# Kernel tuning notes

Hardware: AMD Instinct MI355X
Metric: run time of the kernel (lower is better)

## Reference

```python
import jax, jax.numpy as jnp
import numpy as np

N_NODES = 50000
N_EDGES = 800000
NODE_DIM = 256
EDGE_DIM = 64
NUM_REL = 4
HID = 512      # hidden_dims[0]
LAST = 128     # last_dim_size
BATCH = 16384
EPS = 1e-10    # torchdrug RelationalGraphConv degree-normalization eps


def _glorot(k, shape):
    fan_in = shape[-1]
    return jax.random.normal(k, shape, jnp.float32) / np.sqrt(fan_in).astype(np.float32)


def setup_inputs() -> dict:
    key = jax.random.key(0)
    ks = jax.random.split(key, 20)
    inp = {}
    inp["inputs"] = jax.random.randint(ks[0], (BATCH, 3), 0, N_NODES, dtype=jnp.int32)
    inp["node_feature"] = jax.random.normal(ks[1], (N_NODES, NODE_DIM), jnp.float32)
    inp["edge_feature"] = jax.random.normal(ks[2], (N_EDGES, EDGE_DIM), jnp.float32)
    inp["edge_src"] = jax.random.randint(ks[3], (N_EDGES,), 0, N_NODES, dtype=jnp.int32)
    inp["edge_dst"] = jax.random.randint(ks[4], (N_EDGES,), 0, N_NODES, dtype=jnp.int32)
    inp["edge_rel"] = jax.random.randint(ks[5], (N_EDGES,), 0, NUM_REL, dtype=jnp.int32)
    # RGCN layer 1: 256 -> 512
    inp["We1"] = _glorot(ks[6], (NODE_DIM, EDGE_DIM)); inp["be1"] = jnp.zeros((NODE_DIM,), jnp.float32)
    inp["Wl1"] = _glorot(ks[7], (HID, NUM_REL * NODE_DIM)); inp["bl1"] = jnp.zeros((HID,), jnp.float32)
    inp["Ws1"] = _glorot(ks[8], (HID, NODE_DIM)); inp["bs1"] = jnp.zeros((HID,), jnp.float32)
    # RGCN layer 2: 512 -> 128
    inp["We2"] = _glorot(ks[9], (HID, EDGE_DIM)); inp["be2"] = jnp.zeros((HID,), jnp.float32)
    inp["Wl2"] = _glorot(ks[10], (LAST, NUM_REL * HID)); inp["bl2"] = jnp.zeros((LAST,), jnp.float32)
    inp["Ws2"] = _glorot(ks[11], (LAST, HID)); inp["bs2"] = jnp.zeros((LAST,), jnp.float32)
    # ccle_mlp: edge_dim -> 256 -> 128
    inp["Wc1"] = _glorot(ks[12], (256, EDGE_DIM)); inp["bc1"] = jnp.zeros((256,), jnp.float32)
    inp["Wc2"] = _glorot(ks[13], (LAST, 256)); inp["bc2"] = jnp.zeros((LAST,), jnp.float32)
    # final MLP: 3*128 -> 128 -> 64 -> 1
    inp["Wf1"] = _glorot(ks[14], (128, 3 * LAST)); inp["bf1"] = jnp.zeros((128,), jnp.float32)
    inp["Wf2"] = _glorot(ks[15], (64, 128)); inp["bf2"] = jnp.zeros((64,), jnp.float32)
    inp["Wf3"] = _glorot(ks[16], (1, 64)); inp["bf3"] = jnp.zeros((1,), jnp.float32)
    return inp


def _rgcn_layer(x, edge_src, edge_dst, edge_rel, edge_feat, We, be, Wl, bl, Ws, bs):
    """torchdrug RelationalGraphConv: message = x[src] + edge_linear(edge_feat);
    per-(node,relation) mean aggregation; combine = linear(update) + self_loop(x); relu."""
    in_dim = x.shape[1]
    msg = x[edge_src] + edge_feat @ We.T + be                      # [E, in_dim]
    seg = edge_dst * NUM_REL + edge_rel                            # [E]
    agg = jax.ops.segment_sum(msg, seg, num_segments=N_NODES * NUM_REL)
    cnt = jax.ops.segment_sum(jnp.ones((msg.shape[0], 1), msg.dtype), seg,
                              num_segments=N_NODES * NUM_REL)
    upd = (agg / (cnt + EPS)).reshape(N_NODES, NUM_REL * in_dim)   # [N, R*in_dim]
    return jax.nn.relu(upd @ Wl.T + bl + x @ Ws.T + bs)


def reference(inputs, node_feature, edge_feature, edge_src, edge_dst, edge_rel,
              We1, be1, Wl1, bl1, Ws1, bs1,
              We2, be2, Wl2, bl2, Ws2, bs2,
              Wc1, bc1, Wc2, bc2,
              Wf1, bf1, Wf2, bf2, Wf3, bf3):
    d1, d2, ctx = inputs[:, 0], inputs[:, 1], inputs[:, 2]
    h = _rgcn_layer(node_feature, edge_src, edge_dst, edge_rel, edge_feature,
                    We1, be1, Wl1, bl1, Ws1, bs1)
    h = _rgcn_layer(h, edge_src, edge_dst, edge_rel, edge_feature,
                    We2, be2, Wl2, bl2, Ws2, bs2)
    x1 = h[d1]                                                     # [B, 128]
    x2 = h[d2]                                                     # [B, 128]
    ef = edge_feature[ctx]                                         # [B, 64]
    x3 = jax.nn.relu(ef @ Wc1.T + bc1) @ Wc2.T + bc2               # [B, 128]
    x = jnp.concatenate([x1, x2, x3], axis=1)                      # [B, 384]
    x = jax.nn.relu(x @ Wf1.T + bf1)
    x = jax.nn.relu(x @ Wf2.T + bf2)
    return x @ Wf3.T + bf3                                         # [B, 1]
```

## Files before the change

### kernel.cpp

```cpp
#include <hip/hip_runtime.h>
#include <hip/hip_bf16.h>

#define N_NODES 50000
#define N_EDGES 800000
#define NODE_DIM 256
#define EDGE_DIM 64
#define NUM_REL 4
#define HID 512
#define LAST 128
#define BATCH 16384
#define EPS 1e-10f
#define NSEG (N_NODES * NUM_REL)

#define K1 1600
#define K2 832

typedef __bf16 bf16_t;
typedef __attribute__((ext_vector_type(8))) __bf16 bf16x8;
typedef __attribute__((ext_vector_type(4))) __bf16 bf16x4;
typedef __attribute__((ext_vector_type(2))) __bf16 bf16x2;
typedef __attribute__((ext_vector_type(4))) float f32x4;

typedef __attribute__((address_space(1))) const unsigned int g_u32;
typedef __attribute__((address_space(3))) unsigned int l_u32;
static __device__ __forceinline__ void gload16(const void* g, void* l) {
    __builtin_amdgcn_global_load_lds((g_u32*)g, (l_u32*)l, 16, 0, 0);
}

__global__ __launch_bounds__(256) void hist_kernel(
    const int* __restrict__ edst, const int* __restrict__ erel, int* __restrict__ hist)
{
    int e = blockIdx.x * 256 + threadIdx.x;
    if (e >= N_EDGES) return;
    atomicAdd(&hist[edst[e] * NUM_REL + erel[e]], 1);
}

#define SCAN_B 2048
__global__ __launch_bounds__(256) void scan1(
    const int* __restrict__ in, int* __restrict__ out, int* __restrict__ bsum, int n)
{
    __shared__ int sh[256];
    int base = blockIdx.x * SCAN_B + threadIdx.x * 8;
    int v[8]; int s = 0;
#pragma unroll
    for (int i = 0; i < 8; ++i) {
        int idx = base + i;
        v[i] = s;
        s += (idx < n) ? in[idx] : 0;
    }
    sh[threadIdx.x] = s;
    __syncthreads();
    for (int off = 1; off < 256; off <<= 1) {
        int t = (threadIdx.x >= off) ? sh[threadIdx.x - off] : 0;
        __syncthreads();
        sh[threadIdx.x] += t;
        __syncthreads();
    }
    int texcl = (threadIdx.x == 0) ? 0 : sh[threadIdx.x - 1];
#pragma unroll
    for (int i = 0; i < 8; ++i) {
        int idx = base + i;
        if (idx < n) out[idx] = texcl + v[i];
    }
    if (threadIdx.x == 255) bsum[blockIdx.x] = sh[255];
}

__global__ void scan2(int* bsum, int nb)
{
    if (threadIdx.x == 0 && blockIdx.x == 0) {
        int s = 0;
        for (int i = 0; i < nb; ++i) { int t = bsum[i]; bsum[i] = s; s += t; }
    }
}

__global__ __launch_bounds__(256) void scan3(int* __restrict__ out, int* __restrict__ cursor,
                                             const int* __restrict__ bsum, int n)
{
    int idx = blockIdx.x * SCAN_B + threadIdx.x * 8;
    int add = bsum[blockIdx.x];
#pragma unroll
    for (int i = 0; i < 8; ++i)
        if (idx + i < n) {
            int v = out[idx + i] + add;
            out[idx + i] = v;
            cursor[idx + i] = v;
        }
}

__global__ __launch_bounds__(256) void csr_fill(
    const int* __restrict__ edst, const int* __restrict__ erel, const int* __restrict__ esrc,
    int* __restrict__ cursor,
    int* __restrict__ csr_src, int* __restrict__ csr_eid)
{
    int e = blockIdx.x * 256 + threadIdx.x;
    if (e >= N_EDGES) return;
    int seg = edst[e] * NUM_REL + erel[e];
    int pos = atomicAdd(&cursor[seg], 1);
    csr_src[pos] = esrc[e];
    csr_eid[pos] = e;
}

__global__ __launch_bounds__(256) void prep_small(
    const float* __restrict__ Wc1, const float* __restrict__ Wc2,
    const float* __restrict__ Wf1, const float* __restrict__ Wf2,
    const float* __restrict__ bl1, const float* __restrict__ bs1,
    const float* __restrict__ bl2, const float* __restrict__ bs2,
    bf16_t* __restrict__ Wc1b, bf16_t* __restrict__ Wc2b,
    bf16_t* __restrict__ Wf1b, bf16_t* __restrict__ Wf2b,
    float* __restrict__ bias12, float* __restrict__ bias22)
{
    int i = blockIdx.x * 256 + threadIdx.x;
    const float* src; bf16_t* dst; int base;
    if (i < 4096)        { src = Wc1; dst = Wc1b; base = 0; }
    else if (i < 12288)  { src = Wc2; dst = Wc2b; base = 4096; }
    else if (i < 24576)  { src = Wf1; dst = Wf1b; base = 12288; }
    else if (i < 26624)  { src = Wf2; dst = Wf2b; base = 24576; }
    else {
        int j = i - 26624;
        if (j < 512) bias12[j] = bl1[j] + bs1[j];
        else if (j < 640) bias22[j - 512] = bl2[j - 512] + bs2[j - 512];
        return;
    }
    int k = i - base;
    float4 v = ((const float4*)src)[k];
    bf16x4 o;
    o[0] = (bf16_t)v.x; o[1] = (bf16_t)v.y; o[2] = (bf16_t)v.z; o[3] = (bf16_t)v.w;
    ((bf16x4*)dst)[k] = o;
}

__global__ __launch_bounds__(256) void xconv_k(const float* __restrict__ x, bf16_t* __restrict__ A1,
                                               bf16_t* __restrict__ xb)
{
    int i = blockIdx.x * 256 + threadIdx.x;
    int n = i >> 6;
    int c4 = i & 63;
    float4 v = ((const float4*)(x + (size_t)n * 256))[c4];
    bf16x4 o;
    o[0] = (bf16_t)v.x; o[1] = (bf16_t)v.y; o[2] = (bf16_t)v.z; o[3] = (bf16_t)v.w;
    *(bf16x4*)(A1 + (size_t)n * K1 + 1280 + c4 * 4) = o;
    *(bf16x4*)(xb + (size_t)n * 256 + c4 * 4) = o;
}

__global__ __launch_bounds__(256) void prep_w1cat(
    const float* __restrict__ Wl1, const float* __restrict__ We1,
    const float* __restrict__ Ws1, const float* __restrict__ be1, bf16_t* __restrict__ W1cat)
{
    int j = blockIdx.x;
    int t = threadIdx.x;
    const float* wrow = Wl1 + (size_t)j * 1024;
    bf16_t* out = W1cat + (size_t)j * K1;
    for (int c = t; c < 1024; c += 256) out[c] = (bf16_t)wrow[c];
    {
        int r = t >> 6, e = t & 63;
        float s = 0.f;
        const float* wr = wrow + r * 256;
        for (int c = 0; c < 256; ++c) s += wr[c] * We1[c * 64 + e];
        out[1024 + t] = (bf16_t)s;
    }
    if (t < 256) out[1280 + t] = (bf16_t)Ws1[(size_t)j * 256 + t];
    if (t < 4) {
        float s = 0.f;
        const float* wr = wrow + t * 256;
        for (int c = 0; c < 256; ++c) s += wr[c] * be1[c];
        out[1536 + t] = (bf16_t)s;
    }
    if (t >= 4 && t < 64) out[1536 + t] = (bf16_t)0.f;
}

__global__ __launch_bounds__(256) void prep_w2cat(
    const float* __restrict__ Wl2, const float* __restrict__ We2,
    const float* __restrict__ Ws2, const float* __restrict__ be2, bf16_t* __restrict__ W2cat)
{
    int j = blockIdx.x;
    int t = threadIdx.x;
    const float* wrow = Wl2 + (size_t)j * 2048;
    bf16_t* out = W2cat + (size_t)j * K2;
    {
        int r = t >> 6, e = t & 63;
        float s = 0.f;
        const float* wr = wrow + r * 512;
        for (int k = 0; k < 512; ++k) s += wr[k] * We2[k * 64 + e];
        out[t] = (bf16_t)s;
    }
    for (int c = t; c < 512; c += 256) out[256 + c] = (bf16_t)Ws2[(size_t)j * 512 + c];
    if (t < 4) {
        float s = 0.f;
        const float* wr = wrow + t * 512;
        for (int k = 0; k < 512; ++k) s += wr[k] * be2[k];
        out[768 + t] = (bf16_t)s;
    }
    if (t >= 4 && t < 64) out[768 + t] = (bf16_t)0.f;
}

__global__ __launch_bounds__(256) void prep_w2p(const float* __restrict__ Wl2, bf16_t* __restrict__ W2p)
{
    int idx = blockIdx.x * 256 + threadIdx.x;
    int row = idx >> 9, k = idx & 511;
    int j = row & 127, r = row >> 7;
    W2p[idx] = (bf16_t)Wl2[(size_t)j * 2048 + r * 512 + k];
}

__global__ __launch_bounds__(256) void agg1(
    const float* __restrict__ ef, const bf16_t* __restrict__ xb,
    const int* __restrict__ csr_src, const int* __restrict__ csr_eid,
    const int* __restrict__ offs, const int* __restrict__ hist,
    bf16_t* __restrict__ A1, bf16_t* __restrict__ A2)
{
    int n = blockIdx.x;
    int w = threadIdx.x >> 6;
    int lane = threadIdx.x & 63;
    int half = lane >> 5;
    int l32 = lane & 31;
    int seg = n * NUM_REL + w;
    int beg = offs[seg], ct = hist[seg];

    float xs[8] = {0.f, 0.f, 0.f, 0.f, 0.f, 0.f, 0.f, 0.f};
    float es0 = 0.f, es1 = 0.f;

    int i = 0;
    for (; i + 4 <= ct; i += 4) {
        int sA = csr_src[beg + i + half];
        int sB = csr_src[beg + i + 2 + half];
        int eA = csr_eid[beg + i + half];
        int eB = csr_eid[beg + i + 2 + half];
        bf16x8 vA = *(const bf16x8*)(xb + (size_t)sA * 256 + l32 * 8);
        bf16x8 vB = *(const bf16x8*)(xb + (size_t)sB * 256 + l32 * 8);
        float2 fA = *(const float2*)(ef + (size_t)eA * 64 + l32 * 2);
        float2 fB = *(const float2*)(ef + (size_t)eB * 64 + l32 * 2);
#pragma unroll
        for (int j = 0; j < 8; ++j) xs[j] += (float)vA[j] + (float)vB[j];
        es0 += fA.x + fB.x;
        es1 += fA.y + fB.y;
    }
    for (; i + 2 <= ct; i += 2) {
        int sA = csr_src[beg + i + half];
        int eA = csr_eid[beg + i + half];
        bf16x8 vA = *(const bf16x8*)(xb + (size_t)sA * 256 + l32 * 8);
        float2 fA = *(const float2*)(ef + (size_t)eA * 64 + l32 * 2);
#pragma unroll
        for (int j = 0; j < 8; ++j) xs[j] += (float)vA[j];
        es0 += fA.x;
        es1 += fA.y;
    }
    if (i < ct && half == 0) {
        int sA = csr_src[beg + i];
        int eA = csr_eid[beg + i];
        bf16x8 vA = *(const bf16x8*)(xb + (size_t)sA * 256 + l32 * 8);
        float2 fA = *(const float2*)(ef + (size_t)eA * 64 + l32 * 2);
#pragma unroll
        for (int j = 0; j < 8; ++j) xs[j] += (float)vA[j];
        es0 += fA.x;
        es1 += fA.y;
    }
#pragma unroll
    for (int j = 0; j < 8; ++j) xs[j] += __shfl_xor(xs[j], 32);
    es0 += __shfl_xor(es0, 32);
    es1 += __shfl_xor(es1, 32);

    float inv = 1.0f / ((float)ct + EPS);
    if (half == 0) {
        bf16x8 m;
#pragma unroll
        for (int j = 0; j < 8; ++j) m[j] = (bf16_t)(xs[j] * inv);
        *(bf16x8*)(A1 + (size_t)n * K1 + w * 256 + l32 * 8) = m;
        bf16x2 e2;
        e2[0] = (bf16_t)(es0 * inv);
        e2[1] = (bf16_t)(es1 * inv);
        *(bf16x2*)(A1 + (size_t)n * K1 + 1024 + w * 64 + l32 * 2) = e2;
        *(bf16x2*)(A2 + (size_t)n * K2 + w * 64 + l32 * 2) = e2;
    }
    if (lane == 0) {
        bf16_t fv = (bf16_t)((float)ct * inv);
        A1[(size_t)n * K1 + 1536 + w] = fv;
        A2[(size_t)n * K2 + 768 + w] = fv;
    }
    if (w == 3 && lane >= 4) {
        A1[(size_t)n * K1 + 1536 + lane] = (bf16_t)0.f;
        A2[(size_t)n * K2 + 768 + lane] = (bf16_t)0.f;
    }
}

__global__ __launch_bounds__(256) void agg2(
    const bf16_t* __restrict__ P, const int* __restrict__ csr_src,
    const int* __restrict__ offs, const int* __restrict__ hist,
    float* __restrict__ h2base)
{
    __shared__ float red[4][128];
    int n = blockIdx.x;
    int w = threadIdx.x >> 6;
    int lane = threadIdx.x & 63;
    int half = lane >> 5;
    int l32 = lane & 31;
    int seg = n * NUM_REL + w;
    int beg = offs[seg], ct = hist[seg];

    float s0 = 0.f, s1 = 0.f, s2 = 0.f, s3 = 0.f;
    int i = 0;
    for (; i + 4 <= ct; i += 4) {
        int a = csr_src[beg + i + half];
        int b = csr_src[beg + i + 2 + half];
        bf16x4 va = *(const bf16x4*)(P + (size_t)a * HID + w * 128 + l32 * 4);
        bf16x4 vb = *(const bf16x4*)(P + (size_t)b * HID + w * 128 + l32 * 4);
        s0 += (float)va[0] + (float)vb[0];
        s1 += (float)va[1] + (float)vb[1];
        s2 += (float)va[2] + (float)vb[2];
        s3 += (float)va[3] + (float)vb[3];
    }
    for (; i + 2 <= ct; i += 2) {
        int a = csr_src[beg + i + half];
        bf16x4 va = *(const bf16x4*)(P + (size_t)a * HID + w * 128 + l32 * 4);
        s0 += (float)va[0]; s1 += (float)va[1]; s2 += (float)va[2]; s3 += (float)va[3];
    }
    if (i < ct && half == 0) {
        int a = csr_src[beg + i];
        bf16x4 va = *(const bf16x4*)(P + (size_t)a * HID + w * 128 + l32 * 4);
        s0 += (float)va[0]; s1 += (float)va[1]; s2 += (float)va[2]; s3 += (float)va[3];
    }
    s0 += __shfl_xor(s0, 32);
    s1 += __shfl_xor(s1, 32);
    s2 += __shfl_xor(s2, 32);
    s3 += __shfl_xor(s3, 32);

    float inv = 1.0f / ((float)ct + EPS);
    if (half == 0) {
        red[w][l32 * 4 + 0] = s0 * inv;
        red[w][l32 * 4 + 1] = s1 * inv;
        red[w][l32 * 4 + 2] = s2 * inv;
        red[w][l32 * 4 + 3] = s3 * inv;
    }
    __syncthreads();
    int t = threadIdx.x;
    if (t < 128)
        h2base[(size_t)n * 128 + t] = red[0][t] + red[1][t] + red[2][t] + red[3][t];
}

template<int RELU>
__global__ __launch_bounds__(512) void gemm256(
    const bf16_t* __restrict__ A, int lda,
    const bf16_t* __restrict__ W, int ldw,
    const float* __restrict__ bias,
    bf16_t* __restrict__ Cout, int ldc,
    int M, int N, int K, int ncol)
{
    __shared__ char smem[98304];
    const int tid = threadIdx.x;

    const int nwg = gridDim.x;
    const int q8 = nwg >> 3, r8 = nwg & 7;
    const int xcd = blockIdx.x & 7, li = blockIdx.x >> 3;
    const int wgid = (xcd < r8 ? xcd * (q8 + 1) : r8 * (q8 + 1) + (xcd - r8) * q8) + li;

    const int row0 = (wgid / ncol) * 256;
    const int col0 = (wgid % ncol) * 256;
    const int lane = tid & 63, wv = tid >> 6;

    const int rsub = lane >> 2;
    const int gc = (lane & 3) ^ ((lane >> 3) & 3);
    const bf16_t *pa[2], *pb[2];
    int lof[2];
#pragma unroll
    for (int s = 0; s < 2; ++s) {
        int g = wv * 2 + s;
        int ar = row0 + g * 16 + rsub; if (ar >= M) ar = M - 1;
        int br = col0 + g * 16 + rsub; if (br >= N) br = N - 1;
        pa[s] = A + (size_t)ar * lda + gc * 8;
        pb[s] = W + (size_t)br * ldw + gc * 8;
        lof[s] = g * 1024;
    }

    const int wm = wv >> 2, wn = wv & 3;
    const int r16 = lane & 15, kch = lane >> 4;
    const int slot = (kch ^ ((r16 >> 1) & 3)) << 4;

    f32x4 acc[8][4];
#pragma unroll
    for (int i = 0; i < 8; ++i)
#pragma unroll
        for (int j = 0; j < 4; ++j) acc[i][j] = (f32x4){0.f, 0.f, 0.f, 0.f};

    const int nt = K >> 5;
#pragma unroll
    for (int t = 0; t < 2; ++t) {
        char* b = smem + t * 32768;
        gload16(pa[0] + t * 32, b + lof[0]);
        gload16(pa[1] + t * 32, b + lof[1]);
        gload16(pb[0] + t * 32, b + 16384 + lof[0]);
        gload16(pb[1] + t * 32, b + 16384 + lof[1]);
    }
    asm volatile("s_waitcnt vmcnt(4)" ::: "memory");
    __builtin_amdgcn_s_barrier();

    for (int t = 0; t < nt; ++t) {
        char* buf = smem + (t % 3) * 32768;
        char* nbuf = smem + ((t + 2) % 3) * 32768;
        const bool st = (t + 2 < nt);
        const int k2 = (t + 2) * 32;

        bf16x8 bA[4], bB[4];
#pragma unroll
        for (int i = 0; i < 4; ++i)
            bA[i] = *(const bf16x8*)(buf + (wm * 128 + i * 16 + r16) * 64 + slot);
#pragma unroll
        for (int j = 0; j < 4; ++j)
            bB[j] = *(const bf16x8*)(buf + 16384 + (wn * 64 + j * 16 + r16) * 64 + slot);
        if (st) {
            gload16(pa[0] + k2, nbuf + lof[0]);
            gload16(pa[1] + k2, nbuf + lof[1]);
        }
        __builtin_amdgcn_s_barrier();
        asm volatile("s_waitcnt lgkmcnt(0)" ::: "memory");
        __builtin_amdgcn_sched_barrier(0);
        __builtin_amdgcn_s_setprio(1);
#pragma unroll
        for (int i = 0; i < 4; ++i)
#pragma unroll
            for (int j = 0; j < 4; ++j)
                acc[i][j] = __builtin_amdgcn_mfma_f32_16x16x32_bf16(bA[i], bB[j], acc[i][j], 0, 0, 0);
        __builtin_amdgcn_s_setprio(0);
        __builtin_amdgcn_s_barrier();

        bf16x8 aH[4];
#pragma unroll
        for (int i = 0; i < 4; ++i)
            aH[i] = *(const bf16x8*)(buf + (wm * 128 + 64 + i * 16 + r16) * 64 + slot);
        if (st) {
            gload16(pb[0] + k2, nbuf + 16384 + lof[0]);
            gload16(pb[1] + k2, nbuf + 16384 + lof[1]);
        }
        __builtin_amdgcn_s_barrier();
        asm volatile("s_waitcnt lgkmcnt(0)" ::: "memory");
        __builtin_amdgcn_sched_barrier(0);
        __builtin_amdgcn_s_setprio(1);
#pragma unroll
        for (int i = 0; i < 4; ++i)
#pragma unroll
            for (int j = 0; j < 4; ++j)
                acc[4 + i][j] = __builtin_amdgcn_mfma_f32_16x16x32_bf16(aH[i], bB[j], acc[4 + i][j], 0, 0, 0);
        __builtin_amdgcn_s_setprio(0);
        if (t + 1 < nt) {
            if (st) asm volatile("s_waitcnt vmcnt(4)" ::: "memory");
            else    asm volatile("s_waitcnt vmcnt(0)" ::: "memory");
        }
        __builtin_amdgcn_s_barrier();
    }

    const int crow0 = row0 + wm * 128;
#pragma unroll
    for (int i = 0; i < 8; ++i) {
#pragma unroll
        for (int j = 0; j < 4; ++j) {
            int col = col0 + wn * 64 + j * 16 + r16;
            float bv = bias ? bias[col] : 0.f;
#pragma unroll
            for (int q = 0; q < 4; ++q) {
                int row = crow0 + i * 16 + kch * 4 + q;
                if (row >= M) continue;
                float v = acc[i][j][q] + bv;
                if (RELU) v = fmaxf(v, 0.f);
                Cout[(size_t)row * ldc + col] = (bf16_t)v;
            }
        }
    }
}

template<int RELU, int ACC, int OUTBF>
__global__ __launch_bounds__(256) void gemm_bf16(
    const bf16_t* __restrict__ A, int lda,
    const bf16_t* __restrict__ W, int ldw,
    const float* __restrict__ Cin, int ldcin,
    const float* __restrict__ bias,
    void* __restrict__ Cout, int ldc,
    int M, int N, int K, int ncol)
{
    __shared__ char smem[65536];
    const int tid = threadIdx.x;

    const int nwg = gridDim.x;
    const int q8 = nwg >> 3, r8 = nwg & 7;
    const int xcd = blockIdx.x & 7, li = blockIdx.x >> 3;
    const int wgid = (xcd < r8 ? xcd * (q8 + 1) : r8 * (q8 + 1) + (xcd - r8) * q8) + li;

    const int row0 = (wgid / ncol) * 128;
    const int col0 = (wgid % ncol) * 128;
    const int lane = tid & 63, wv = tid >> 6;

    const int rsub = lane >> 3;
    const int gchunk = (lane & 7) ^ rsub;
    const bf16_t* pa[4]; const bf16_t* pb[4];
    int lofs[4];
#pragma unroll
    for (int s = 0; s < 4; ++s) {
        int q = wv * 4 + s;
        int ar = row0 + q * 8 + rsub; if (ar >= M) ar = M - 1;
        int br = col0 + q * 8 + rsub; if (br >= N) br = N - 1;
        pa[s] = A + (size_t)ar * lda + gchunk * 8;
        pb[s] = W + (size_t)br * ldw + gchunk * 8;
        lofs[s] = q * 1024;
    }

    const int wm = wv >> 1, wn = wv & 1;
    const int r16 = lane & 15, kch = lane >> 4;
    const int sw = r16 & 7;

    f32x4 acc[4][4];
#pragma unroll
    for (int i = 0; i < 4; ++i)
#pragma unroll
        for (int j = 0; j < 4; ++j) acc[i][j] = (f32x4){0.f, 0.f, 0.f, 0.f};

#pragma unroll
    for (int s = 0; s < 4; ++s) {
        gload16(pa[s], smem + lofs[s]);
        gload16(pb[s], smem + 16384 + lofs[s]);
    }

    const int nk = K >> 6;
    int cur = 0;
    for (int it = 0; it < nk; ++it) {
        const int k0 = it << 6;
        if (it + 1 < nk) {
            char* nb = smem + ((cur ^ 1) << 15);
#pragma unroll
            for (int s = 0; s < 4; ++s) {
                gload16(pa[s] + k0 + 64, nb + lofs[s]);
                gload16(pb[s] + k0 + 64, nb + 16384 + lofs[s]);
            }
            asm volatile("s_waitcnt vmcnt(8)" ::: "memory");
        } else {
            asm volatile("s_waitcnt vmcnt(0)" ::: "memory");
        }
        __builtin_amdgcn_s_barrier();
        __builtin_amdgcn_sched_barrier(0);
        const char* As = smem + (cur << 15);
        const char* Bs = As + 16384;
#pragma unroll
        for (int t = 0; t < 2; ++t) {
            const int slot = ((t * 4 + kch) ^ sw) << 4;
            bf16x8 af[4], bfm[4];
#pragma unroll
            for (int i = 0; i < 4; ++i)
                af[i] = *(const bf16x8*)(As + (wm * 64 + i * 16 + r16) * 128 + slot);
#pragma unroll
            for (int j = 0; j < 4; ++j)
                bfm[j] = *(const bf16x8*)(Bs + (wn * 64 + j * 16 + r16) * 128 + slot);
#pragma unroll
            for (int i = 0; i < 4; ++i)
#pragma unroll
                for (int j = 0; j < 4; ++j)
                    acc[i][j] = __builtin_amdgcn_mfma_f32_16x16x32_bf16(af[i], bfm[j], acc[i][j], 0, 0, 0);
        }
        __builtin_amdgcn_s_barrier();
        cur ^= 1;
    }

    const int crow0 = row0 + wm * 64;
#pragma unroll
    for (int i = 0; i < 4; ++i) {
#pragma unroll
        for (int j = 0; j < 4; ++j) {
            int col = col0 + wn * 64 + j * 16 + r16;
            if (col >= N) continue;
            float bv = bias ? bias[col] : 0.f;
#pragma unroll
            for (int q = 0; q < 4; ++q) {
                int row = crow0 + i * 16 + kch * 4 + q;
                if (row >= M) continue;
                float v = acc[i][j][q] + bv;
                if (ACC) v += Cin[(size_t)row * ldcin + col];
                if (RELU) v = fmaxf(v, 0.f);
                if (OUTBF) ((bf16_t*)Cout)[(size_t)row * ldc + col] = (bf16_t)v;
                else       ((float*)Cout)[(size_t)row * ldc + col] = v;
            }
        }
    }
}

__global__ __launch_bounds__(256) void gemm_f1g(
    const int* __restrict__ inputs, const bf16_t* __restrict__ h2,
    const bf16_t* __restrict__ x3, const bf16_t* __restrict__ Wf1b,
    const float* __restrict__ bf1, bf16_t* __restrict__ f1)
{
    __shared__ char smem[65536];
    const int tid = threadIdx.x;
    const int nwg = gridDim.x;
    const int q8 = nwg >> 3;
    const int xcd = blockIdx.x & 7, li = blockIdx.x >> 3;
    const int wgid = xcd * q8 + li;
    const int row0 = wgid * 128;
    const int lane = tid & 63, wv = tid >> 6;

    const int rsub = lane >> 3;
    const int gchunk = (lane & 7) ^ rsub;
    const bf16_t* baseA[4][3];
    const bf16_t* pb[4];
    int lofs[4];
#pragma unroll
    for (int s = 0; s < 4; ++s) {
        int q = wv * 4 + s;
        int ar = row0 + q * 8 + rsub;
        int d1 = inputs[ar * 3 + 0];
        int d2 = inputs[ar * 3 + 1];
        baseA[s][0] = h2 + (size_t)d1 * 128 + gchunk * 8;
        baseA[s][1] = h2 + (size_t)d2 * 128 + gchunk * 8;
        baseA[s][2] = x3 + (size_t)ar * 128 + gchunk * 8;
        int br = q * 8 + rsub;
        pb[s] = Wf1b + (size_t)br * 384 + gchunk * 8;
        lofs[s] = q * 1024;
    }

    const int wm = wv >> 1, wn = wv & 1;
    const int r16 = lane & 15, kch = lane >> 4;
    const int sw = r16 & 7;

    f32x4 acc[4][4];
#pragma unroll
    for (int i = 0; i < 4; ++i)
#pragma unroll
        for (int j = 0; j < 4; ++j) acc[i][j] = (f32x4){0.f, 0.f, 0.f, 0.f};

#pragma unroll
    for (int s = 0; s < 4; ++s) {
        gload16(baseA[s][0], smem + lofs[s]);
        gload16(pb[s], smem + 16384 + lofs[s]);
    }

    int cur = 0;
#pragma unroll
    for (int it = 0; it < 6; ++it) {
        const int k0 = it << 6;
        if (it < 5) {
            const int kn = k0 + 64;
            const int reg = kn >> 7, off = kn & 127;
            char* nb = smem + ((cur ^ 1) << 15);
#pragma unroll
            for (int s = 0; s < 4; ++s) {
                gload16(baseA[s][reg] + off, nb + lofs[s]);
                gload16(pb[s] + kn, nb + 16384 + lofs[s]);
            }
            asm volatile("s_waitcnt vmcnt(8)" ::: "memory");
        } else {
            asm volatile("s_waitcnt vmcnt(0)" ::: "memory");
        }
        __builtin_amdgcn_s_barrier();
        __builtin_amdgcn_sched_barrier(0);
        const char* As = smem + (cur << 15);
        const char* Bs = As + 16384;
#pragma unroll
        for (int t = 0; t < 2; ++t) {
            const int slot = ((t * 4 + kch) ^ sw) << 4;
            bf16x8 af[4], bfm[4];
#pragma unroll
            for (int i = 0; i < 4; ++i)
                af[i] = *(const bf16x8*)(As + (wm * 64 + i * 16 + r16) * 128 + slot);
#pragma unroll
            for (int j = 0; j < 4; ++j)
                bfm[j] = *(const bf16x8*)(Bs + (wn * 64 + j * 16 + r16) * 128 + slot);
#pragma unroll
            for (int i = 0; i < 4; ++i)
#pragma unroll
                for (int j = 0; j < 4; ++j)
                    acc[i][j] = __builtin_amdgcn_mfma_f32_16x16x32_bf16(af[i], bfm[j], acc[i][j], 0, 0, 0);
        }
        __builtin_amdgcn_s_barrier();
        cur ^= 1;
    }

    const int crow0 = row0 + wm * 64;
#pragma unroll
    for (int i = 0; i < 4; ++i) {
#pragma unroll
        for (int j = 0; j < 4; ++j) {
            int col = wn * 64 + j * 16 + r16;
            float bv = bf1[col];
#pragma unroll
            for (int q = 0; q < 4; ++q) {
                int row = crow0 + i * 16 + kch * 4 + q;
                float v = fmaxf(acc[i][j][q] + bv, 0.f);
                f1[(size_t)row * 128 + col] = (bf16_t)v;
            }
        }
    }
}

__global__ __launch_bounds__(256) void gather_ef(
    const int* __restrict__ inputs, const float* __restrict__ ef, bf16_t* __restrict__ ef_g)
{
    int i = blockIdx.x * 256 + threadIdx.x;
    int row = i >> 4, c4 = i & 15;
    int ctx = inputs[row * 3 + 2];
    float4 v = *(const float4*)(ef + (size_t)ctx * 64 + c4 * 4);
    bf16x4 o;
    o[0] = (bf16_t)v.x; o[1] = (bf16_t)v.y; o[2] = (bf16_t)v.z; o[3] = (bf16_t)v.w;
    *(bf16x4*)(ef_g + (size_t)row * 64 + c4 * 4) = o;
}

__global__ __launch_bounds__(256) void head_tail(
    const bf16_t* __restrict__ f1, const bf16_t* __restrict__ Wf2b,
    const float* __restrict__ bf2, const float* __restrict__ Wf3,
    const float* __restrict__ bf3, float* __restrict__ out)
{
    __shared__ bf16_t sf1[128 * 128];
    int blk = blockIdx.x;
    int tid = threadIdx.x;
    const bf16_t* gsrc = f1 + (size_t)blk * 128 * 128;
    for (int i = tid; i < 128 * 16; i += 256)
        ((bf16x8*)sf1)[i] = ((const bf16x8*)gsrc)[i];
    int lane = tid & 63, wv = tid >> 6;
    bf16x8 w[16];
#pragma unroll
    for (int c = 0; c < 16; ++c) w[c] = ((const bf16x8*)(Wf2b + lane * 128))[c];
    float bias2 = bf2[lane];
    float wf3 = Wf3[lane];
    float b3 = bf3[0];
    __syncthreads();
    for (int r = wv; r < 128; r += 4) {
        const bf16x8* frow = (const bf16x8*)(sf1 + r * 128);
        float acc = 0.f;
#pragma unroll
        for (int c = 0; c < 16; ++c) {
            bf16x8 fv = frow[c];
#pragma unroll
            for (int j = 0; j < 8; ++j) acc += (float)fv[j] * (float)w[c][j];
        }
        float v = fmaxf(acc + bias2, 0.f) * wf3;
#pragma unroll
        for (int off = 32; off > 0; off >>= 1) v += __shfl_down(v, off);
        if (lane == 0) out[blk * 128 + r] = v + b3;
    }
}

extern "C" void kernel_launch(void* const* d_in, const int* in_sizes, int n_in,
                              void* d_out, int out_size, void* d_ws, size_t ws_size,
                              hipStream_t stream)
{
    const int*   inputs       = (const int*)  d_in[0];
    const float* node_feature = (const float*)d_in[1];
    const float* edge_feature = (const float*)d_in[2];
    const int*   edge_src     = (const int*)  d_in[3];
    const int*   edge_dst     = (const int*)  d_in[4];
    const int*   edge_rel     = (const int*)  d_in[5];
    const float* We1 = (const float*)d_in[6];
    const float* be1 = (const float*)d_in[7];
    const float* Wl1 = (const float*)d_in[8];
    const float* bl1 = (const float*)d_in[9];
    const float* Ws1 = (const float*)d_in[10];
    const float* bs1 = (const float*)d_in[11];
    const float* We2 = (const float*)d_in[12];
    const float* be2 = (const float*)d_in[13];
    const float* Wl2 = (const float*)d_in[14];
    const float* bl2 = (const float*)d_in[15];
    const float* Ws2 = (const float*)d_in[16];
    const float* bs2 = (const float*)d_in[17];
    const float* Wc1 = (const float*)d_in[18];
    const float* bc1 = (const float*)d_in[19];
    const float* Wc2 = (const float*)d_in[20];
    const float* bc2 = (const float*)d_in[21];
    const float* Wf1 = (const float*)d_in[22];
    const float* bf1 = (const float*)d_in[23];
    const float* Wf2 = (const float*)d_in[24];
    const float* bf2 = (const float*)d_in[25];
    const float* Wf3 = (const float*)d_in[26];
    const float* bf3 = (const float*)d_in[27];
    float* out = (float*)d_out;

    char* p = (char*)d_ws;
    auto alloc = [&](size_t bytes) { char* r = p; p += (bytes + 255) & ~(size_t)255; return r; };
    int* hist     = (int*)alloc(NSEG * 4);
    int* offs     = (int*)alloc(NSEG * 4);
    int* cursor   = (int*)alloc(NSEG * 4);
    int* csr_src  = (int*)alloc(N_EDGES * 4);
    int* csr_eid  = (int*)alloc(N_EDGES * 4);
    int* bsums    = (int*)alloc(128 * 4);
    bf16_t* A1    = (bf16_t*)alloc((size_t)N_NODES * K1 * 2);
    bf16_t* A2    = (bf16_t*)alloc((size_t)N_NODES * K2 * 2);
    bf16_t* xb    = (bf16_t*)alloc((size_t)N_NODES * 256 * 2);
    bf16_t* Pbuf  = (bf16_t*)alloc((size_t)N_NODES * HID * 2);
    float*  h2base= (float*)alloc((size_t)N_NODES * 128 * 4);
    bf16_t* h2    = (bf16_t*)alloc((size_t)N_NODES * 128 * 2);
    bf16_t* W1cat = (bf16_t*)alloc((size_t)512 * K1 * 2);
    bf16_t* W2cat = (bf16_t*)alloc((size_t)128 * K2 * 2);
    bf16_t* W2p   = (bf16_t*)alloc((size_t)512 * 512 * 2);
    bf16_t* Wc1b  = (bf16_t*)alloc(256 * 64 * 2);
    bf16_t* Wc2b  = (bf16_t*)alloc(128 * 256 * 2);
    bf16_t* Wf1b  = (bf16_t*)alloc(128 * 384 * 2);
    bf16_t* Wf2b  = (bf16_t*)alloc(64 * 128 * 2);
    float*  bias12= (float*)alloc(512 * 4);
    float*  bias22= (float*)alloc(128 * 4);
    bf16_t* ef_g  = (bf16_t*)alloc((size_t)BATCH * 64 * 2);
    bf16_t* u3    = (bf16_t*)alloc((size_t)BATCH * 256 * 2);
    bf16_t* x3buf = (bf16_t*)alloc((size_t)BATCH * 128 * 2);
    bf16_t* f1    = (bf16_t*)alloc((size_t)BATCH * 128 * 2);

    hipMemsetAsync(hist, 0, NSEG * 4, stream);
    hist_kernel<<<(N_EDGES + 255) / 256, 256, 0, stream>>>(edge_dst, edge_rel, hist);
    int nscan = (NSEG + SCAN_B - 1) / SCAN_B;
    scan1<<<nscan, 256, 0, stream>>>(hist, offs, bsums, NSEG);
    scan2<<<1, 64, 0, stream>>>(bsums, nscan);
    scan3<<<nscan, 256, 0, stream>>>(offs, cursor, bsums, NSEG);
    csr_fill<<<(N_EDGES + 255) / 256, 256, 0, stream>>>(edge_dst, edge_rel, edge_src,
                                                        cursor, csr_src, csr_eid);

    prep_w1cat<<<512, 256, 0, stream>>>(Wl1, We1, Ws1, be1, W1cat);
    prep_w2cat<<<128, 256, 0, stream>>>(Wl2, We2, Ws2, be2, W2cat);
    prep_w2p<<<(512 * 512) / 256, 256, 0, stream>>>(Wl2, W2p);
    prep_small<<<(26624 + 640 + 255) / 256, 256, 0, stream>>>(
        Wc1, Wc2, Wf1, Wf2, bl1, bs1, bl2, bs2,
        Wc1b, Wc2b, Wf1b, Wf2b, bias12, bias22);
    xconv_k<<<(N_NODES * 64 + 255) / 256, 256, 0, stream>>>(node_feature, A1, xb);

    agg1<<<N_NODES, 256, 0, stream>>>(edge_feature, xb, csr_src, csr_eid, offs, hist, A1, A2);
    {
        int nrow = (N_NODES + 255) / 256, ncol = HID / 256;
        gemm256<1><<<nrow * ncol, 512, 0, stream>>>(A1, K1, W1cat, K1, bias12,
                                                    A2 + 256, K2, N_NODES, HID, K1, ncol);
    }

    {
        int nrow = (N_NODES + 255) / 256, ncol = HID / 256;
        gemm256<0><<<nrow * ncol, 512, 0, stream>>>(A2 + 256, K2, W2p, 512, nullptr,
                                                    Pbuf, HID, N_NODES, HID, 512, ncol);
    }
    agg2<<<N_NODES, 256, 0, stream>>>(Pbuf, csr_src, offs, hist, h2base);
    {
        int nrow = (N_NODES + 127) / 128;
        gemm_bf16<1, 1, 1><<<nrow, 256, 0, stream>>>(A2, K2, W2cat, K2, h2base, 128, bias22,
                                                     h2, 128, N_NODES, 128, K2, 1);
    }

    gather_ef<<<(BATCH * 16) / 256, 256, 0, stream>>>(inputs, edge_feature, ef_g);
    {
        gemm_bf16<1, 0, 1><<<(BATCH / 128) * 2, 256, 0, stream>>>(ef_g, 64, Wc1b, 64, nullptr, 0, bc1,
                                                                  u3, 256, BATCH, 256, 64, 2);
    }
    {
        gemm_bf16<0, 0, 1><<<BATCH / 128, 256, 0, stream>>>(u3, 256, Wc2b, 256, nullptr, 0, bc2,
                                                            x3buf, 128, BATCH, 128, 256, 1);
    }
    gemm_f1g<<<BATCH / 128, 256, 0, stream>>>(inputs, h2, x3buf, Wf1b, bf1, f1);
    head_tail<<<BATCH / 128, 256, 0, stream>>>(f1, Wf2b, bf2, Wf3, bf3, out);
}
```

Measured before the change: 692.2 us.

## Balance edge aggregation across warps with shared-memory atomic accumulation

The agg1 and agg2 kernels now split all of a node's incoming edges evenly over eight 32-lane groups, instead of giving one wavefront to each relation. Each group looks up an edge's relation from segment boundaries and adds into per-relation shared-memory accumulators with atomics, using a lane-based swizzle to spread bank conflicts. The goal is to remove load imbalance when relation degrees are uneven and to keep more gathers in flight. The cost is LDS atomic traffic and contention, plus non-deterministic float summation order.

```diff
diff --git a/kernel.cpp b/kernel.cpp
--- a/kernel.cpp
+++ b/kernel.cpp
@@ -206,77 +206,59 @@
     const int* __restrict__ offs, const int* __restrict__ hist,
     bf16_t* __restrict__ A1, bf16_t* __restrict__ A2)
 {
+    __shared__ float accX[4][256];
+    __shared__ float accE[4][64];
+    __shared__ int sb[8];
     int n = blockIdx.x;
-    int w = threadIdx.x >> 6;
-    int lane = threadIdx.x & 63;
-    int half = lane >> 5;
-    int l32 = lane & 31;
-    int seg = n * NUM_REL + w;
-    int beg = offs[seg], ct = hist[seg];
-
-    float xs[8] = {0.f, 0.f, 0.f, 0.f, 0.f, 0.f, 0.f, 0.f};
-    float es0 = 0.f, es1 = 0.f;
-
-    int i = 0;
-    for (; i + 4 <= ct; i += 4) {
-        int sA = csr_src[beg + i + half];
-        int sB = csr_src[beg + i + 2 + half];
-        int eA = csr_eid[beg + i + half];
-        int eB = csr_eid[beg + i + 2 + half];
-        bf16x8 vA = *(const bf16x8*)(xb + (size_t)sA * 256 + l32 * 8);
-        bf16x8 vB = *(const bf16x8*)(xb + (size_t)sB * 256 + l32 * 8);
-        float2 fA = *(const float2*)(ef + (size_t)eA * 64 + l32 * 2);
-        float2 fB = *(const float2*)(ef + (size_t)eB * 64 + l32 * 2);
-#pragma unroll
-        for (int j = 0; j < 8; ++j) xs[j] += (float)vA[j] + (float)vB[j];
-        es0 += fA.x + fB.x;
-        es1 += fA.y + fB.y;
-    }
-    for (; i + 2 <= ct; i += 2) {
-        int sA = csr_src[beg + i + half];
-        int eA = csr_eid[beg + i + half];
-        bf16x8 vA = *(const bf16x8*)(xb + (size_t)sA * 256 + l32 * 8);
-        float2 fA = *(const float2*)(ef + (size_t)eA * 64 + l32 * 2);
-#pragma unroll
-        for (int j = 0; j < 8; ++j) xs[j] += (float)vA[j];
-        es0 += fA.x;
-        es1 += fA.y;
-    }
-    if (i < ct && half == 0) {
-        int sA = csr_src[beg + i];
-        int eA = csr_eid[beg + i];
-        bf16x8 vA = *(const bf16x8*)(xb + (size_t)sA * 256 + l32 * 8);
-        float2 fA = *(const float2*)(ef + (size_t)eA * 64 + l32 * 2);
-#pragma unroll
-        for (int j = 0; j < 8; ++j) xs[j] += (float)vA[j];
-        es0 += fA.x;
-        es1 += fA.y;
-    }
-#pragma unroll
-    for (int j = 0; j < 8; ++j) xs[j] += __shfl_xor(xs[j], 32);
-    es0 += __shfl_xor(es0, 32);
-    es1 += __shfl_xor(es1, 32);
-
-    float inv = 1.0f / ((float)ct + EPS);
-    if (half == 0) {
-        bf16x8 m;
-#pragma unroll
-        for (int j = 0; j < 8; ++j) m[j] = (bf16_t)(xs[j] * inv);
-        *(bf16x8*)(A1 + (size_t)n * K1 + w * 256 + l32 * 8) = m;
-        bf16x2 e2;
-        e2[0] = (bf16_t)(es0 * inv);
-        e2[1] = (bf16_t)(es1 * inv);
-        *(bf16x2*)(A1 + (size_t)n * K1 + 1024 + w * 64 + l32 * 2) = e2;
-        *(bf16x2*)(A2 + (size_t)n * K2 + w * 64 + l32 * 2) = e2;
-    }
-    if (lane == 0) {
-        bf16_t fv = (bf16_t)((float)ct * inv);
-        A1[(size_t)n * K1 + 1536 + w] = fv;
-        A2[(size_t)n * K2 + 768 + w] = fv;
-    }
-    if (w == 3 && lane >= 4) {
-        A1[(size_t)n * K1 + 1536 + lane] = (bf16_t)0.f;
-        A2[(size_t)n * K2 + 768 + lane] = (bf16_t)0.f;
+    int tid = threadIdx.x;
+    for (int i = tid; i < 4 * 256; i += 256) ((float*)accX)[i] = 0.f;
+    if (tid < 4 * 64) ((float*)accE)[tid] = 0.f;
+    if (tid < 4) sb[tid] = offs[n * 4 + tid];
+    if (tid == 4) sb[4] = offs[n * 4 + 3] + hist[n * 4 + 3];
+    __syncthreads();
+    const int beg = sb[0], b1 = sb[1], b2 = sb[2], b3 = sb[3], end = sb[4];
+    const int grp = tid >> 5, l32 = tid & 31;
+    const int sw8 = l32 >> 2;
+
+    for (int j = beg + grp; j < end; j += 8) {
+        int src = csr_src[j];
+        int e = csr_eid[j];
+        int r = (j >= b1) + (j >= b2) + (j >= b3);
+        bf16x8 v = *(const bf16x8*)(xb + (size_t)src * 256 + l32 * 8);
+        float2 f = *(const float2*)(ef + (size_t)e * 64 + l32 * 2);
+        float* ax = &accX[r][l32 * 8];
+#pragma unroll
+        for (int q = 0; q < 8; ++q) {
+            int qq = q ^ sw8;
+            atomicAdd(&ax[qq], (float)v[qq]);
+        }
+        float* ae = &accE[r][l32 * 2];
+        atomicAdd(&ae[0], f.x);
+        atomicAdd(&ae[1], f.y);
+    }
+    __syncthreads();
+
+    int cts[4] = {b1 - beg, b2 - b1, b3 - b2, end - b3};
+    float inv[4];
+#pragma unroll
+    for (int r = 0; r < 4; ++r) inv[r] = 1.f / ((float)cts[r] + EPS);
+
+#pragma unroll
+    for (int r = 0; r < 4; ++r)
+        A1[(size_t)n * K1 + r * 256 + tid] = (bf16_t)(accX[r][tid] * inv[r]);
+    {
+        int r = tid >> 6, c = tid & 63;
+        bf16_t ev = (bf16_t)(accE[r][c] * inv[r]);
+        A1[(size_t)n * K1 + 1024 + tid] = ev;
+        A2[(size_t)n * K2 + tid] = ev;
+    }
+    if (tid < 4) {
+        bf16_t fb = (bf16_t)((float)cts[tid] * inv[tid]);
+        A1[(size_t)n * K1 + 1536 + tid] = fb;
+        A2[(size_t)n * K2 + 768 + tid] = fb;
+    } else if (tid < 64) {
+        A1[(size_t)n * K1 + 1536 + tid] = (bf16_t)0.f;
+        A2[(size_t)n * K2 + 768 + tid] = (bf16_t)0.f;
     }
 }
 
@@ -285,53 +267,37 @@
     const int* __restrict__ offs, const int* __restrict__ hist,
     float* __restrict__ h2base)
 {
-    __shared__ float red[4][128];
+    __shared__ float accP[4][128];
+    __shared__ int sb[8];
     int n = blockIdx.x;
-    int w = threadIdx.x >> 6;
-    int lane = threadIdx.x & 63;
-    int half = lane >> 5;
-    int l32 = lane & 31;
-    int seg = n * NUM_REL + w;
-    int beg = offs[seg], ct = hist[seg];
-
-    float s0 = 0.f, s1 = 0.f, s2 = 0.f, s3 = 0.f;
-    int i = 0;
-    for (; i + 4 <= ct; i += 4) {
-        int a = csr_src[beg + i + half];
-        int b = csr_src[beg + i + 2 + half];
-        bf16x4 va = *(const bf16x4*)(P + (size_t)a * HID + w * 128 + l32 * 4);
-        bf16x4 vb = *(const bf16x4*)(P + (size_t)b * HID + w * 128 + l32 * 4);
-        s0 += (float)va[0] + (float)vb[0];
-        s1 += (float)va[1] + (float)vb[1];
-        s2 += (float)va[2] + (float)vb[2];
-        s3 += (float)va[3] + (float)vb[3];
-    }
-    for (; i + 2 <= ct; i += 2) {
-        int a = csr_src[beg + i + half];
-        bf16x4 va = *(const bf16x4*)(P + (size_t)a * HID + w * 128 + l32 * 4);
-        s0 += (float)va[0]; s1 += (float)va[1]; s2 += (float)va[2]; s3 += (float)va[3];
-    }
-    if (i < ct && half == 0) {
-        int a = csr_src[beg + i];
-        bf16x4 va = *(const bf16x4*)(P + (size_t)a * HID + w * 128 + l32 * 4);
-        s0 += (float)va[0]; s1 += (float)va[1]; s2 += (float)va[2]; s3 += (float)va[3];
-    }
-    s0 += __shfl_xor(s0, 32);
-    s1 += __shfl_xor(s1, 32);
-    s2 += __shfl_xor(s2, 32);
-    s3 += __shfl_xor(s3, 32);
-
-    float inv = 1.0f / ((float)ct + EPS);
-    if (half == 0) {
-        red[w][l32 * 4 + 0] = s0 * inv;
-        red[w][l32 * 4 + 1] = s1 * inv;
-        red[w][l32 * 4 + 2] = s2 * inv;
-        red[w][l32 * 4 + 3] = s3 * inv;
-    }
+    int tid = threadIdx.x;
+    for (int i = tid; i < 512; i += 256) ((float*)accP)[i] = 0.f;
+    if (tid < 4) sb[tid] = offs[n * 4 + tid];
+    if (tid == 4) sb[4] = offs[n * 4 + 3] + hist[n * 4 + 3];
     __syncthreads();
-    int t = threadIdx.x;
-    if (t < 128)
-        h2base[(size_t)n * 128 + t] = red[0][t] + red[1][t] + red[2][t] + red[3][t];
+    const int beg = sb[0], b1 = sb[1], b2 = sb[2], b3 = sb[3], end = sb[4];
+    const int grp = tid >> 5, l32 = tid & 31;
+    const int sw4 = (l32 >> 3) & 3;
+
+    for (int j = beg + grp; j < end; j += 8) {
+        int src = csr_src[j];
+        int r = (j >= b1) + (j >= b2) + (j >= b3);
+        bf16x4 v = *(const bf16x4*)(P + (size_t)src * HID + r * 128 + l32 * 4);
+        float* ap = &accP[r][l32 * 4];
+#pragma unroll
+        for (int q = 0; q < 4; ++q) {
+            int qq = q ^ sw4;
+            atomicAdd(&ap[qq], (float)v[qq]);
+        }
+    }
+    __syncthreads();
+    if (tid < 128) {
+        float c0 = (float)(b1 - beg), c1 = (float)(b2 - b1);
+        float c2 = (float)(b3 - b2), c3 = (float)(end - b3);
+        float s = accP[0][tid] / (c0 + EPS) + accP[1][tid] / (c1 + EPS)
+                + accP[2][tid] / (c2 + EPS) + accP[3][tid] / (c3 + EPS);
+        h2base[(size_t)n * 128 + tid] = s;
+    }
 }
 
 template<int RELU>
```

After: 2.340 ms. 3.38x slower.

## Switch GEMM to BK=64 double-buffered pipeline with 8-chunk XOR swizzle

Applied to the files above, without the earlier changes.

Restructures the 256x256 bf16 GEMM main loop from a triple-buffered K=32 tile with split A/B loads into a double-buffered K=64 tile using 128 KB of LDS. Each iteration now waits once, runs two k-substeps of 32 MFMAs each, and issues the next-next tile's loads after a trailing barrier. The LDS layout changes to 128-byte rows with an 8-way XOR swizzle. The aim is fewer barriers and waits per unit of K and larger global loads per stage, at the cost of doubled LDS (limits occupancy) and less fine-grained overlap of loads with MFMA.

```diff
diff --git a/kernel.cpp b/kernel.cpp
--- a/kernel.cpp
+++ b/kernel.cpp
@@ -342,7 +342,7 @@
     bf16_t* __restrict__ Cout, int ldc,
     int M, int N, int K, int ncol)
 {
-    __shared__ char smem[98304];
+    __shared__ char smem[131072];
     const int tid = threadIdx.x;
 
     const int nwg = gridDim.x;
@@ -354,23 +354,23 @@
     const int col0 = (wgid % ncol) * 256;
     const int lane = tid & 63, wv = tid >> 6;
 
-    const int rsub = lane >> 2;
-    const int gc = (lane & 3) ^ ((lane >> 3) & 3);
-    const bf16_t *pa[2], *pb[2];
-    int lof[2];
-#pragma unroll
-    for (int s = 0; s < 2; ++s) {
-        int g = wv * 2 + s;
-        int ar = row0 + g * 16 + rsub; if (ar >= M) ar = M - 1;
-        int br = col0 + g * 16 + rsub; if (br >= N) br = N - 1;
-        pa[s] = A + (size_t)ar * lda + gc * 8;
-        pb[s] = W + (size_t)br * ldw + gc * 8;
-        lof[s] = g * 1024;
+    const int srow = tid >> 3;
+    const int slot8 = tid & 7;
+    const int gch = slot8 ^ (srow & 7);
+    const bf16_t* pa[4]; const bf16_t* pb[4];
+    int lof[4];
+#pragma unroll
+    for (int i = 0; i < 4; ++i) {
+        int r = srow + i * 64;
+        int ar = row0 + r; if (ar >= M) ar = M - 1;
+        int br = col0 + r; if (br >= N) br = N - 1;
+        pa[i] = A + (size_t)ar * lda + gch * 8;
+        pb[i] = W + (size_t)br * ldw + gch * 8;
+        lof[i] = r * 128 + slot8 * 16;
     }
 
     const int wm = wv >> 2, wn = wv & 3;
     const int r16 = lane & 15, kch = lane >> 4;
-    const int slot = (kch ^ ((r16 >> 1) & 3)) << 4;
 
     f32x4 acc[8][4];
 #pragma unroll
@@ -378,70 +378,56 @@
 #pragma unroll
         for (int j = 0; j < 4; ++j) acc[i][j] = (f32x4){0.f, 0.f, 0.f, 0.f};
 
-    const int nt = K >> 5;
-#pragma unroll
-    for (int t = 0; t < 2; ++t) {
-        char* b = smem + t * 32768;
-        gload16(pa[0] + t * 32, b + lof[0]);
-        gload16(pa[1] + t * 32, b + lof[1]);
-        gload16(pb[0] + t * 32, b + 16384 + lof[0]);
-        gload16(pb[1] + t * 32, b + 16384 + lof[1]);
-    }
-    asm volatile("s_waitcnt vmcnt(4)" ::: "memory");
-    __builtin_amdgcn_s_barrier();
+    const int nt = K >> 6;
+#pragma unroll
+    for (int tt = 0; tt < 2; ++tt) {
+        char* b = smem + tt * 65536;
+#pragma unroll
+        for (int i = 0; i < 4; ++i) {
+            gload16(pa[i] + tt * 64, b + lof[i]);
+            gload16(pb[i] + tt * 64, b + 32768 + lof[i]);
+        }
+    }
 
     for (int t = 0; t < nt; ++t) {
-        char* buf = smem + (t % 3) * 32768;
-        char* nbuf = smem + ((t + 2) % 3) * 32768;
-        const bool st = (t + 2 < nt);
-        const int k2 = (t + 2) * 32;
-
-        bf16x8 bA[4], bB[4];
-#pragma unroll
-        for (int i = 0; i < 4; ++i)
-            bA[i] = *(const bf16x8*)(buf + (wm * 128 + i * 16 + r16) * 64 + slot);
-#pragma unroll
-        for (int j = 0; j < 4; ++j)
-            bB[j] = *(const bf16x8*)(buf + 16384 + (wn * 64 + j * 16 + r16) * 64 + slot);
-        if (st) {
-            gload16(pa[0] + k2, nbuf + lof[0]);
-            gload16(pa[1] + k2, nbuf + lof[1]);
-        }
+        if (t + 1 < nt) asm volatile("s_waitcnt vmcnt(8)" ::: "memory");
+        else            asm volatile("s_waitcnt vmcnt(0)" ::: "memory");
         __builtin_amdgcn_s_barrier();
-        asm volatile("s_waitcnt lgkmcnt(0)" ::: "memory");
         __builtin_amdgcn_sched_barrier(0);
-        __builtin_amdgcn_s_setprio(1);
-#pragma unroll
-        for (int i = 0; i < 4; ++i)
-#pragma unroll
-            for (int j = 0; j < 4; ++j)
-                acc[i][j] = __builtin_amdgcn_mfma_f32_16x16x32_bf16(bA[i], bB[j], acc[i][j], 0, 0, 0);
-        __builtin_amdgcn_s_setprio(0);
+        const char* As = smem + (t & 1) * 65536;
+        const char* Bs = As + 32768;
+#pragma unroll
+        for (int ks = 0; ks < 2; ++ks) {
+            bf16x8 bB[4], aF[8];
+#pragma unroll
+            for (int j = 0; j < 4; ++j) {
+                int r = wn * 64 + j * 16 + r16;
+                bB[j] = *(const bf16x8*)(Bs + r * 128 + (((ks * 4 + kch) ^ (r & 7)) << 4));
+            }
+#pragma unroll
+            for (int i = 0; i < 8; ++i) {
+                int r = wm * 128 + i * 16 + r16;
+                aF[i] = *(const bf16x8*)(As + r * 128 + (((ks * 4 + kch) ^ (r & 7)) << 4));
+            }
+            asm volatile("s_waitcnt lgkmcnt(0)" ::: "memory");
+            __builtin_amdgcn_sched_barrier(0);
+            __builtin_amdgcn_s_setprio(1);
+#pragma unroll
+            for (int i = 0; i < 8; ++i)
+#pragma unroll
+                for (int j = 0; j < 4; ++j)
+                    acc[i][j] = __builtin_amdgcn_mfma_f32_16x16x32_bf16(aF[i], bB[j], acc[i][j], 0, 0, 0);
+            __builtin_amdgcn_s_setprio(0);
+        }
         __builtin_amdgcn_s_barrier();
-
-        bf16x8 aH[4];
-#pragma unroll
-        for (int i = 0; i < 4; ++i)
-            aH[i] = *(const bf16x8*)(buf + (wm * 128 + 64 + i * 16 + r16) * 64 + slot);
-        if (st) {
-            gload16(pb[0] + k2, nbuf + 16384 + lof[0]);
-            gload16(pb[1] + k2, nbuf + 16384 + lof[1]);
-        }
-        __builtin_amdgcn_s_barrier();
-        asm volatile("s_waitcnt lgkmcnt(0)" ::: "memory");
-        __builtin_amdgcn_sched_barrier(0);
-        __builtin_amdgcn_s_setprio(1);
-#pragma unroll
-        for (int i = 0; i < 4; ++i)
-#pragma unroll
-            for (int j = 0; j < 4; ++j)
-                acc[4 + i][j] = __builtin_amdgcn_mfma_f32_16x16x32_bf16(aH[i], bB[j], acc[4 + i][j], 0, 0, 0);
-        __builtin_amdgcn_s_setprio(0);
-        if (t + 1 < nt) {
-            if (st) asm volatile("s_waitcnt vmcnt(4)" ::: "memory");
-            else    asm volatile("s_waitcnt vmcnt(0)" ::: "memory");
-        }
-        __builtin_amdgcn_s_barrier();
+        if (t + 2 < nt) {
+            char* nb = smem + (t & 1) * 65536;
+#pragma unroll
+            for (int i = 0; i < 4; ++i) {
+                gload16(pa[i] + (t + 2) * 64, nb + lof[i]);
+                gload16(pb[i] + (t + 2) * 64, nb + 32768 + lof[i]);
+            }
+        }
     }
 
     const int crow0 = row0 + wm * 128;
```

New measurement: 698.9 us. Within noise of the previous version (+1.0%).
